# Performance work log

Hardware: AMD Instinct MI355X
Metric: run time of the kernel (lower is better)

Reference implementation:

```python
import jax, jax.numpy as jnp
import numpy as np

B, S, V = 8, 8192, 64
D, DV, DT, H = 256, 32, 256, 8
DH = D // H

def setup_inputs() -> dict:
    key = jax.random.key(0)
    ks = jax.random.split(key, 24)
    def p(i, shape, s=0.02):
        return jax.random.normal(ks[i], shape, jnp.float32) * s
    return {
        'times': jax.random.uniform(ks[0], (B, S), jnp.float32),
        'feature_ids': jax.random.randint(ks[1], (B, S), 0, V),
        'values': jax.random.normal(ks[2], (B, S), jnp.float32),
        'valid_mask': jax.random.randint(ks[3], (B, S), 0, 2).astype(bool),
        'me_w': p(4, (D,), 1.0), 'me_b': p(5, (D,)),
        'var_emb': p(6, (V, DV), 1.0),
        'time_w': p(7, (DT,), 1.0), 'time_b': p(8, (DT,)),
        'agg_w': p(9, (D + DT, D - DV)), 'agg_b': p(10, (D - DV,)),
        'wq': p(11, (D, D)), 'bq': p(12, (D,)),
        'wk': p(13, (D, D)), 'bk': p(14, (D,)),
        'wv': p(15, (D, D)), 'bv': p(16, (D,)),
        'wo': p(17, (D, D)), 'bo': p(18, (D,)),
        'cw1': p(19, (D, D)), 'cb1': p(20, (D,)),
        'cw2': p(21, (D, 1)), 'cb2': p(22, (1,)),
    }

def reference(times, feature_ids, values, valid_mask,
              me_w, me_b, var_emb, time_w, time_b, agg_w, agg_b,
              wq, bq, wk, bk, wv, bv, wo, bo, cw1, cb1, cw2, cb2):
    # Embeddings: measurement [B,S,D], variate [B,S,DV], time [B,S,DT]
    e_l = values[..., None] * me_w + me_b
    v_l = var_emb[feature_ids]
    u_l = times[..., None] * time_w + time_b
    eu = jnp.concatenate([e_l, u_l], axis=-1)                   # [B,S,D+DT]
    h_l = jnp.concatenate([v_l, eu @ agg_w + agg_b], axis=-1)   # [B,S,D]

    # Vectorized masked segment mean per variate (replaces Python loop)
    var_mask = (feature_ids[:, None, :] == jnp.arange(V)[None, :, None]) \
               & valid_mask[:, None, :]                         # [B,V,S] bool
    mf = var_mask.astype(h_l.dtype)
    sums = jnp.einsum('bvs,bsd->bvd', mf, h_l)
    counts = jnp.clip(mf.sum(-1), 1.0)                          # [B,V]
    f_mean = sums / counts[..., None]                           # [B,V,D]

    # Grouped cross-attention: one query per variate, shared K/V = h_l
    kpm = ~var_mask                                             # key padding mask
    all_masked = ~var_mask.any(-1)                              # [B,V]
    kpm = kpm.at[:, :, 0].set(kpm[:, :, 0] & ~all_masked)       # unmask pos 0 if empty

    q = (f_mean @ wq + bq).reshape(B, V, H, DH)
    k = (h_l @ wk + bk).reshape(B, S, H, DH)
    v = (h_l @ wv + bv).reshape(B, S, H, DH)
    scores = jnp.einsum('bvhd,bshd->bvhs', q, k) / np.sqrt(DH)  # [B,V,H,S]
    neg = jnp.finfo(scores.dtype).min
    scores = jnp.where(kpm[:, :, None, :], neg, scores)
    attn = jax.nn.softmax(scores, axis=-1)
    ctx = jnp.einsum('bvhs,bshd->bvhd', attn, v).reshape(B, V, D)
    f_var = ctx @ wo + bo                                       # [B,V,D]

    f = f_var.mean(axis=1)                                      # [B,D]
    out = jax.nn.relu(f @ cw1 + cb1) @ cw2 + cb2                # [B,1]
    return out
```

## Files before the change

### kernel.cpp

```cpp
#include <hip/hip_runtime.h>
#include <hip/hip_bf16.h>
#include <math.h>

#define BB 8
#define SS 8192
#define VV 64
#define AGG_OUT 224

#define WS_FLAGS 0
#define WS_A     16
#define WS_C     240
#define WS_D     464
#define WS_AQ    688
#define WS_CQ    944
#define WS_DQ    1200
#define WS_AK    1456
#define WS_CK    1712
#define WS_DK    1968
#define WS_AV    2224
#define WS_CV    2480
#define WS_DV    2736
#define WS_WQE   2992
#define WS_WKE   19376
#define WS_WVE   35760
#define WS_CSUM  52144
#define WS_BINS  54192
#define WS_COEF  66480
#define WS_SP    82864
#define WS_ACC   148416
#define WS_CNT   148424

__device__ __forceinline__ float ldf(const void* p, int idx, int fm) {
  if (fm) {
    unsigned int u = ((const unsigned short*)p)[idx];
    return __uint_as_float(u << 16);
  }
  return ((const float*)p)[idx];
}

__device__ __forceinline__ bool mask_at(const void* p, int idx, int mm) {
  switch (mm) {
    case 0: return ((const int*)p)[idx] != 0;
    case 1: return ((const float*)p)[idx] != 0.0f;
    case 2: return ((const unsigned short*)p)[idx] != 0;
    default: return ((const unsigned char*)p)[idx] != 0;
  }
}

__device__ __forceinline__ unsigned int fkey(float f) {
  unsigned int u = __float_as_uint(f);
  return (u & 0x80000000u) ? ~u : (u | 0x80000000u);
}
__device__ __forceinline__ float funkey(unsigned int k) {
  unsigned int u = (k & 0x80000000u) ? (k ^ 0x80000000u) : ~k;
  return __uint_as_float(u);
}

__device__ __forceinline__ int detect_fm_block(const void* times) {
  __shared__ int cntR;
  int tid = threadIdx.x;
  if (tid == 0) cntR = 0;
  __syncthreads();
  const unsigned int* tw = (const unsigned int*)times;
  int local = 0;
  for (int i = tid; i < 1024; i += 256) {
    unsigned int lo = tw[i] & 0xFFFFu;
    if (lo >= 0x3800u && lo < 0x3F80u) local++;
  }
  atomicAdd(&cntR, local);
  __syncthreads();
  int r = (cntR > 512) ? 1 : 0;
  __syncthreads();
  return r;
}

__device__ __forceinline__ int detect_mm_block(const void* mask) {
  __shared__ int f01, ff32, fbf;
  int tid = threadIdx.x;
  if (tid == 0) { f01 = 1; ff32 = 1; fbf = 1; }
  __syncthreads();
  const unsigned int* mw = (const unsigned int*)mask;
  int l01 = 1, lf32 = 1, lbf = 1;
  for (int i = tid; i < 2048; i += 256) {
    unsigned int w = mw[i];
    if (w > 1u) l01 = 0;
    if (!(w == 0u || w == 0x3F800000u)) lf32 = 0;
    unsigned int h0 = w & 0xFFFFu, h1 = w >> 16;
    if (!((h0 == 0u || h0 == 0x3F80u) && (h1 == 0u || h1 == 0x3F80u))) lbf = 0;
  }
  if (!l01) atomicAnd(&f01, 0);
  if (!lf32) atomicAnd(&ff32, 0);
  if (!lbf) atomicAnd(&fbf, 0);
  __syncthreads();
  int r = f01 ? 0 : (ff32 ? 1 : (fbf ? 2 : 3));
  __syncthreads();
  return r;
}

__global__ void __launch_bounds__(256) k_front(const void* times, const void* values,
                                               const int* fids, const void* mask,
                                               const void* me_w, const void* me_b,
                                               const void* time_w, const void* time_b,
                                               const void* agg_w, const void* agg_b,
                                               float* ws) {
  int blk = blockIdx.x, tid = threadIdx.x;
  if (blk < 224) {
    int fm = detect_fm_block(times);
    int j = blk, i = tid;
    float w0 = ldf(agg_w, i * AGG_OUT + j, fm);
    float w1 = ldf(agg_w, (256 + i) * AGG_OUT + j, fm);
    float sa = ldf(me_w, i, fm) * w0;
    float sc = ldf(time_w, i, fm) * w1;
    float sd = ldf(me_b, i, fm) * w0 + ldf(time_b, i, fm) * w1;
    #pragma unroll
    for (int off = 32; off >= 1; off >>= 1) {
      sa += __shfl_xor(sa, off);
      sc += __shfl_xor(sc, off);
      sd += __shfl_xor(sd, off);
    }
    __shared__ float r[3][4];
    int wid = i >> 6;
    if ((i & 63) == 0) { r[0][wid] = sa; r[1][wid] = sc; r[2][wid] = sd; }
    __syncthreads();
    if (i == 0) {
      ws[WS_A + j] = r[0][0] + r[0][1] + r[0][2] + r[0][3];
      ws[WS_C + j] = r[1][0] + r[1][1] + r[1][2] + r[1][3];
      ws[WS_D + j] = r[2][0] + r[2][1] + r[2][2] + r[2][3] + ldf(agg_b, j, fm);
    }
  } else if (blk < 352) {
    int fm = detect_fm_block(times);
    int mm = detect_mm_block(mask);
    int sblk = blk - 224, b = sblk >> 4, chunk = sblk & 15;
    __shared__ float hc[64], hsv[64], hst[64];
    __shared__ unsigned int hvn[64], hvx[64], htn[64], htx[64];
    if (tid < 64) {
      hc[tid] = 0.f; hsv[tid] = 0.f; hst[tid] = 0.f;
      hvn[tid] = 0xFFFFFFFFu; hvx[tid] = 0u;
      htn[tid] = 0xFFFFFFFFu; htx[tid] = 0u;
    }
    __syncthreads();
    #pragma unroll
    for (int k = 0; k < 2; k++) {
      int idx = b * SS + chunk * 512 + k * 256 + tid;
      if (mask_at(mask, idx, mm)) {
        int f = fids[idx];
        float val = ldf(values, idx, fm), tim = ldf(times, idx, fm);
        atomicAdd(&hc[f], 1.0f);
        atomicAdd(&hsv[f], val);
        atomicAdd(&hst[f], tim);
        unsigned int vk = fkey(val), tk = fkey(tim);
        atomicMin(&hvn[f], vk); atomicMax(&hvx[f], vk);
        atomicMin(&htn[f], tk); atomicMax(&htx[f], tk);
      }
    }
    __syncthreads();
    if (tid < 64) {
      int base = WS_SP + (sblk * 64 + tid) * 8;
      ws[base + 0] = hc[tid];
      ws[base + 1] = hsv[tid];
      ws[base + 2] = hst[tid];
      ((unsigned int*)ws)[base + 3] = hvn[tid];
      ((unsigned int*)ws)[base + 4] = hvx[tid];
      ((unsigned int*)ws)[base + 5] = htn[tid];
      ((unsigned int*)ws)[base + 6] = htx[tid];
    }
  } else {
    int zblk = blk - 352;
    for (int i = zblk * 256 + tid; i < 14336; i += 2048) ws[WS_CSUM + i] = 0.f;
    if (zblk == 1 && tid < 16) ws[WS_ACC + tid] = 0.f;
    if (zblk == 0) {
      int fm = detect_fm_block(times);
      int mm = detect_mm_block(mask);
      if (tid == 0) { ((int*)ws)[0] = fm; ((int*)ws)[1] = mm; }
    }
  }
}

__global__ void __launch_bounds__(256) k_pre(const void* wq, const void* wk,
                                             const void* wv, const void* bk,
                                             const void* bv, const void* var_emb,
                                             float* ws) {
  int fm = ((const int*)ws)[0];
  int blk = blockIdx.x, tid = threadIdx.x;
  if (blk < 24) {
    int X = blk >> 3, dg = blk & 7;
    const void* w = (X == 0) ? wq : (X == 1) ? wk : wv;
    __shared__ float sha[224], shc[224], shd[224];
    if (tid < 224) {
      sha[tid] = ws[WS_A + tid];
      shc[tid] = ws[WS_C + tid];
      shd[tid] = ws[WS_D + tid];
    }
    __syncthreads();
    int dsub = tid & 31, jg = tid >> 5;
    int d = dg * 32 + dsub;
    float sa = 0.f, sc = 0.f, sd = 0.f;
    #pragma unroll 4
    for (int jj = 0; jj < 28; jj++) {
      int j = jg * 28 + jj;
      float ww = ldf(w, (32 + j) * 256 + d, fm);
      sa += sha[j] * ww; sc += shc[j] * ww; sd += shd[j] * ww;
    }
    __shared__ float ps[3][8][32];
    ps[0][jg][dsub] = sa; ps[1][jg][dsub] = sc; ps[2][jg][dsub] = sd;
    __syncthreads();
    if (tid < 32) {
      float ra = 0.f, rc = 0.f, rd = 0.f;
      #pragma unroll
      for (int g = 0; g < 8; g++) {
        ra += ps[0][g][tid]; rc += ps[1][g][tid]; rd += ps[2][g][tid];
      }
      int dd = dg * 32 + tid;
      if (X == 1) rd += ldf(bk, dd, fm);
      if (X == 2) rd += ldf(bv, dd, fm);
      int base = (X == 0) ? WS_AQ : (X == 1) ? WS_AK : WS_AV;
      ws[base + dd] = ra;
      ws[base + 256 + dd] = rc;
      ws[base + 512 + dd] = rd;
    }
  } else {
    int idx = blk - 24, X = idx >> 6, v = idx & 63, d = tid;
    const void* w = (X == 0) ? wq : (X == 1) ? wk : wv;
    float s = 0.f;
    #pragma unroll 8
    for (int i = 0; i < 32; i++)
      s += ldf(var_emb, v * 32 + i, fm) * ldf(w, i * 256 + d, fm);
    int base = (X == 0) ? WS_WQE : (X == 1) ? WS_WKE : WS_WVE;
    ws[base + v * 256 + d] = s;
  }
}

__global__ void __launch_bounds__(256) k_coef(const void* values, const void* times,
                                              const int* fids, const void* bq,
                                              float* ws) {
  int fm = ((const int*)ws)[0];
  int bv = blockIdx.x, b = bv >> 6, v = bv & 63;
  int tid = threadIdx.x, h = tid >> 5;
  __shared__ float sp[16][8];
  if (tid < 128) {
    int sl = tid >> 3, c = tid & 7;
    sp[sl][c] = ws[WS_SP + ((b * 16 + sl) * 64 + v) * 8 + c];
  }
  __syncthreads();
  float cT = 0.f, svT = 0.f, stT = 0.f;
  unsigned int vnk = 0xFFFFFFFFu, vxk = 0u, tnk = 0xFFFFFFFFu, txk = 0u;
  #pragma unroll
  for (int sl = 0; sl < 16; sl++) {
    cT += sp[sl][0]; svT += sp[sl][1]; stT += sp[sl][2];
    unsigned int a3 = __float_as_uint(sp[sl][3]);
    unsigned int a4 = __float_as_uint(sp[sl][4]);
    unsigned int a5 = __float_as_uint(sp[sl][5]);
    unsigned int a6 = __float_as_uint(sp[sl][6]);
    vnk = min(vnk, a3); vxk = max(vxk, a4);
    tnk = min(tnk, a5); txk = max(txk, a6);
  }
  if (cT == 0.f) {
    int f0 = fids[b * SS];
    float v0 = ldf(values, b * SS, fm), t0 = ldf(times, b * SS, fm);
    float ctx = ws[WS_WVE + f0 * 256 + tid] + ws[WS_DV + tid]
              + v0 * ws[WS_AV + tid] + t0 * ws[WS_CV + tid];
    atomicAdd(&ws[WS_CSUM + b * 256 + tid], ctx);
    return;
  }
  float inv = 1.0f / cT, mv = svT * inv, mt = stT * inv;
  float qv = ldf(bq, tid, fm) + ws[WS_WQE + v * 256 + tid]
           + mv * ws[WS_AQ + tid] + mt * ws[WS_CQ + tid] + ws[WS_DQ + tid];
  qv *= 0.17677669529663687f * 1.4426950408889634f;
  float pA = qv * (ws[WS_WKE + v * 256 + tid] + ws[WS_DK + tid]);
  float pB = qv * ws[WS_AK + tid];
  float pC = qv * ws[WS_CK + tid];
  #pragma unroll
  for (int off = 16; off >= 1; off >>= 1) {
    pA += __shfl_xor(pA, off);
    pB += __shfl_xor(pB, off);
    pC += __shfl_xor(pC, off);
  }
  if ((tid & 31) == 0) {
    float vmn = funkey(vnk), vmx = funkey(vxk);
    float tmn = funkey(tnk), tmx = funkey(txk);
    float m = pA + fmaxf(pB * vmn, pB * vmx) + fmaxf(pC * tmn, pC * tmx);
    int base = WS_COEF + (bv * 8 + h) * 4;
    ws[base + 0] = pA; ws[base + 1] = pB; ws[base + 2] = pC; ws[base + 3] = m;
  }
}

__global__ void __launch_bounds__(256) k_accum(const void* values, const void* times,
                                               const int* fids, const void* mask,
                                               float* ws) {
  int fm = ((const int*)ws)[0], mm = ((const int*)ws)[1];
  int blk = blockIdx.x, tid = threadIdx.x;
  int b = blk >> 5, chunk = blk & 31;
  __shared__ float co[64 * 36];
  __shared__ float bins[64 * 25];
  for (int i = tid; i < 2048; i += 256) {
    int v = i >> 5, r = i & 31;
    co[v * 36 + r] = ws[WS_COEF + b * 2048 + i];
  }
  for (int i = tid; i < 1600; i += 256) bins[i] = 0.f;
  __syncthreads();
  {
    int idx = b * SS + chunk * 256 + tid;
    if (mask_at(mask, idx, mm)) {
      int f = fids[idx];
      float val = ldf(values, idx, fm), tim = ldf(times, idx, fm);
      #pragma unroll
      for (int h = 0; h < 8; h++) {
        int cb = f * 36 + h * 4;
        float w = exp2f(co[cb] + val * co[cb + 1] + tim * co[cb + 2] - co[cb + 3]);
        int bb = f * 25 + h * 3;
        atomicAdd(&bins[bb], w);
        atomicAdd(&bins[bb + 1], w * val);
        atomicAdd(&bins[bb + 2], w * tim);
      }
    }
  }
  __syncthreads();
  for (int i = tid; i < 1536; i += 256) {
    int f = i / 24, r = i - f * 24;
    float x = bins[f * 25 + r];
    if (x != 0.f) atomicAdd(&ws[WS_BINS + b * 1536 + i], x);
  }
}

__global__ void __launch_bounds__(1024) k_fin(const void* wo, const void* bo,
                                              const void* cw1, const void* cb1,
                                              const void* cw2, const void* cb2,
                                              float* ws, void* out) {
  int fm = ((const int*)ws)[0];
  int b = blockIdx.x, tid = threadIdx.x;
  __shared__ float aa[64][9], tt[64][9], ne[64];
  __shared__ float ps[4][256], cs[256], fv[256], pr[16];
  if (tid < 512) {
    int v = tid >> 3, h = tid & 7;
    int base = WS_BINS + b * 1536 + v * 24 + h * 3;
    float W = ws[base], WV = ws[base + 1], WT = ws[base + 2];
    float iW = (W > 0.f) ? 1.0f / W : 0.f;
    aa[v][h] = WV * iW; tt[v][h] = WT * iW;
    if (h == 0) ne[v] = (W > 0.f) ? 1.f : 0.f;
  }
  __syncthreads();
  int d = tid & 255, vg = tid >> 8, h = d >> 5;
  float accP = 0.f, accA = 0.f, accT = 0.f, accN = 0.f;
  #pragma unroll 4
  for (int k = 0; k < 16; k++) {
    int v = vg * 16 + k;
    float nef = ne[v];
    accP += nef * ws[WS_WVE + v * 256 + d];
    accA += aa[v][h];
    accT += tt[v][h];
    accN += nef;
  }
  ps[vg][d] = accP + accN * ws[WS_DV + d] + accA * ws[WS_AV + d] + accT * ws[WS_CV + d];
  __syncthreads();
  if (tid < 256)
    cs[tid] = (ws[WS_CSUM + b * 256 + tid] + ps[0][tid] + ps[1][tid]
             + ps[2][tid] + ps[3][tid]) * (1.0f / 64.0f);
  __syncthreads();
  float s = 0.f;
  #pragma unroll 8
  for (int k = 0; k < 64; k++) {
    int i = vg * 64 + k;
    s += cs[i] * ldf(wo, i * 256 + d, fm);
  }
  ps[vg][d] = s;
  __syncthreads();
  if (tid < 256) fv[tid] = ps[0][tid] + ps[1][tid] + ps[2][tid] + ps[3][tid]
                         + ldf(bo, tid, fm);
  __syncthreads();
  float t2 = 0.f;
  #pragma unroll 8
  for (int k = 0; k < 64; k++) {
    int i = vg * 64 + k;
    t2 += fv[i] * ldf(cw1, i * 256 + d, fm);
  }
  ps[vg][d] = t2;
  __syncthreads();
  float p = 0.f;
  if (tid < 256) {
    float t = ps[0][tid] + ps[1][tid] + ps[2][tid] + ps[3][tid] + ldf(cb1, tid, fm);
    t = fmaxf(t, 0.f);
    p = t * ldf(cw2, tid, fm);
  }
  #pragma unroll
  for (int off = 32; off >= 1; off >>= 1) p += __shfl_xor(p, off);
  if ((tid & 63) == 0) pr[tid >> 6] = p;
  __syncthreads();
  if (tid == 0) {
    float o = ldf(cb2, 0, fm);
    #pragma unroll
    for (int wgi = 0; wgi < 16; wgi++) o += pr[wgi];
    if (fm) {
      unsigned int x = __float_as_uint(o);
      unsigned int r = (x + 0x7FFFu + ((x >> 16) & 1u)) >> 16;
      ((unsigned short*)out)[b] = (unsigned short)r;
    } else {
      ((float*)out)[b] = o;
    }
  }
}

extern "C" void kernel_launch(void* const* d_in, const int* in_sizes, int n_in,
                              void* d_out, int out_size, void* d_ws, size_t ws_size,
                              hipStream_t stream) {
  const void* times   = d_in[0];
  const int*  fids    = (const int*)d_in[1];
  const void* values  = d_in[2];
  const void* vmask   = d_in[3];
  const void* me_w    = d_in[4];
  const void* me_b    = d_in[5];
  const void* var_emb = d_in[6];
  const void* time_w  = d_in[7];
  const void* time_b  = d_in[8];
  const void* agg_w   = d_in[9];
  const void* agg_b   = d_in[10];
  const void* wq = d_in[11]; const void* bq = d_in[12];
  const void* wk = d_in[13]; const void* bk = d_in[14];
  const void* wv = d_in[15]; const void* bv = d_in[16];
  const void* wo = d_in[17]; const void* bo = d_in[18];
  const void* cw1 = d_in[19]; const void* cb1 = d_in[20];
  const void* cw2 = d_in[21]; const void* cb2 = d_in[22];
  float* ws = (float*)d_ws;

  k_front<<<360, 256, 0, stream>>>(times, values, fids, vmask,
                                   me_w, me_b, time_w, time_b, agg_w, agg_b, ws);
  k_pre<<<216, 256, 0, stream>>>(wq, wk, wv, bk, bv, var_emb, ws);
  k_coef<<<512, 256, 0, stream>>>(values, times, fids, bq, ws);
  k_accum<<<256, 256, 0, stream>>>(values, times, fids, vmask, ws);
  k_fin<<<8, 1024, 0, stream>>>(wo, bo, cw1, cb1, cw2, cb2, ws, d_out);
}
```

Measured before the change: 142.1 us.

## Rebalance work across kernels: move var-emb projections to front, precompute PVE in coef

The var_emb×W projection blocks move from k_pre into k_front, so they run alongside the stats and aggregation blocks, and k_pre shrinks to 24 blocks. The per-batch nonempty-variate sum over WVE, previously computed in the serial 8-block k_fin, is now computed by 8 extra k_coef blocks from the partial counts. k_accum also loads coefficients with float4. The goal is to shorten the critical path in small kernels and the tail kernel. k_front gains more work, and each new block calls detect_fm_block redundantly.

Result: no change. 142.8 us (+0.6%).

```diff
diff --git a/kernel.cpp b/kernel.cpp
--- a/kernel.cpp
+++ b/kernel.cpp
@@ -27,8 +27,7 @@
 #define WS_BINS  54192
 #define WS_COEF  66480
 #define WS_SP    82864
-#define WS_ACC   148416
-#define WS_CNT   148424
+#define WS_PVE   148416
 
 __device__ __forceinline__ float ldf(const void* p, int idx, int fm) {
   if (fm) {
@@ -102,6 +101,8 @@
                                                const void* me_w, const void* me_b,
                                                const void* time_w, const void* time_b,
                                                const void* agg_w, const void* agg_b,
+                                               const void* wq, const void* wk,
+                                               const void* wv, const void* var_emb,
                                                float* ws) {
   int blk = blockIdx.x, tid = threadIdx.x;
   if (blk < 224) {
@@ -164,62 +165,17 @@
       ((unsigned int*)ws)[base + 5] = htn[tid];
       ((unsigned int*)ws)[base + 6] = htx[tid];
     }
-  } else {
+  } else if (blk < 360) {
     int zblk = blk - 352;
     for (int i = zblk * 256 + tid; i < 14336; i += 2048) ws[WS_CSUM + i] = 0.f;
-    if (zblk == 1 && tid < 16) ws[WS_ACC + tid] = 0.f;
     if (zblk == 0) {
       int fm = detect_fm_block(times);
       int mm = detect_mm_block(mask);
       if (tid == 0) { ((int*)ws)[0] = fm; ((int*)ws)[1] = mm; }
     }
-  }
-}
-
-__global__ void __launch_bounds__(256) k_pre(const void* wq, const void* wk,
-                                             const void* wv, const void* bk,
-                                             const void* bv, const void* var_emb,
-                                             float* ws) {
-  int fm = ((const int*)ws)[0];
-  int blk = blockIdx.x, tid = threadIdx.x;
-  if (blk < 24) {
-    int X = blk >> 3, dg = blk & 7;
-    const void* w = (X == 0) ? wq : (X == 1) ? wk : wv;
-    __shared__ float sha[224], shc[224], shd[224];
-    if (tid < 224) {
-      sha[tid] = ws[WS_A + tid];
-      shc[tid] = ws[WS_C + tid];
-      shd[tid] = ws[WS_D + tid];
-    }
-    __syncthreads();
-    int dsub = tid & 31, jg = tid >> 5;
-    int d = dg * 32 + dsub;
-    float sa = 0.f, sc = 0.f, sd = 0.f;
-    #pragma unroll 4
-    for (int jj = 0; jj < 28; jj++) {
-      int j = jg * 28 + jj;
-      float ww = ldf(w, (32 + j) * 256 + d, fm);
-      sa += sha[j] * ww; sc += shc[j] * ww; sd += shd[j] * ww;
-    }
-    __shared__ float ps[3][8][32];
-    ps[0][jg][dsub] = sa; ps[1][jg][dsub] = sc; ps[2][jg][dsub] = sd;
-    __syncthreads();
-    if (tid < 32) {
-      float ra = 0.f, rc = 0.f, rd = 0.f;
-      #pragma unroll
-      for (int g = 0; g < 8; g++) {
-        ra += ps[0][g][tid]; rc += ps[1][g][tid]; rd += ps[2][g][tid];
-      }
-      int dd = dg * 32 + tid;
-      if (X == 1) rd += ldf(bk, dd, fm);
-      if (X == 2) rd += ldf(bv, dd, fm);
-      int base = (X == 0) ? WS_AQ : (X == 1) ? WS_AK : WS_AV;
-      ws[base + dd] = ra;
-      ws[base + 256 + dd] = rc;
-      ws[base + 512 + dd] = rd;
-    }
   } else {
-    int idx = blk - 24, X = idx >> 6, v = idx & 63, d = tid;
+    int fm = detect_fm_block(times);
+    int idx = blk - 360, X = idx >> 6, v = idx & 63, d = tid;
     const void* w = (X == 0) ? wq : (X == 1) ? wk : wv;
     float s = 0.f;
     #pragma unroll 8
@@ -230,57 +186,130 @@
   }
 }
 
+__global__ void __launch_bounds__(256) k_pre(const void* wq, const void* wk,
+                                             const void* wv, const void* bk,
+                                             const void* bv, float* ws) {
+  int fm = ((const int*)ws)[0];
+  int blk = blockIdx.x, tid = threadIdx.x;
+  int X = blk >> 3, dg = blk & 7;
+  const void* w = (X == 0) ? wq : (X == 1) ? wk : wv;
+  __shared__ float sha[224], shc[224], shd[224];
+  if (tid < 224) {
+    sha[tid] = ws[WS_A + tid];
+    shc[tid] = ws[WS_C + tid];
+    shd[tid] = ws[WS_D + tid];
+  }
+  __syncthreads();
+  int dsub = tid & 31, jg = tid >> 5;
+  int d = dg * 32 + dsub;
+  float sa = 0.f, sc = 0.f, sd = 0.f;
+  #pragma unroll 4
+  for (int jj = 0; jj < 28; jj++) {
+    int j = jg * 28 + jj;
+    float ww = ldf(w, (32 + j) * 256 + d, fm);
+    sa += sha[j] * ww; sc += shc[j] * ww; sd += shd[j] * ww;
+  }
+  __shared__ float ps[3][8][32];
+  ps[0][jg][dsub] = sa; ps[1][jg][dsub] = sc; ps[2][jg][dsub] = sd;
+  __syncthreads();
+  if (tid < 32) {
+    float ra = 0.f, rc = 0.f, rd = 0.f;
+    #pragma unroll
+    for (int g = 0; g < 8; g++) {
+      ra += ps[0][g][tid]; rc += ps[1][g][tid]; rd += ps[2][g][tid];
+    }
+    int dd = dg * 32 + tid;
+    if (X == 1) rd += ldf(bk, dd, fm);
+    if (X == 2) rd += ldf(bv, dd, fm);
+    int base = (X == 0) ? WS_AQ : (X == 1) ? WS_AK : WS_AV;
+    ws[base + dd] = ra;
+    ws[base + 256 + dd] = rc;
+    ws[base + 512 + dd] = rd;
+  }
+}
+
 __global__ void __launch_bounds__(256) k_coef(const void* values, const void* times,
                                               const int* fids, const void* bq,
                                               float* ws) {
   int fm = ((const int*)ws)[0];
-  int bv = blockIdx.x, b = bv >> 6, v = bv & 63;
-  int tid = threadIdx.x, h = tid >> 5;
-  __shared__ float sp[16][8];
-  if (tid < 128) {
-    int sl = tid >> 3, c = tid & 7;
-    sp[sl][c] = ws[WS_SP + ((b * 16 + sl) * 64 + v) * 8 + c];
-  }
-  __syncthreads();
-  float cT = 0.f, svT = 0.f, stT = 0.f;
-  unsigned int vnk = 0xFFFFFFFFu, vxk = 0u, tnk = 0xFFFFFFFFu, txk = 0u;
-  #pragma unroll
-  for (int sl = 0; sl < 16; sl++) {
-    cT += sp[sl][0]; svT += sp[sl][1]; stT += sp[sl][2];
-    unsigned int a3 = __float_as_uint(sp[sl][3]);
-    unsigned int a4 = __float_as_uint(sp[sl][4]);
-    unsigned int a5 = __float_as_uint(sp[sl][5]);
-    unsigned int a6 = __float_as_uint(sp[sl][6]);
-    vnk = min(vnk, a3); vxk = max(vxk, a4);
-    tnk = min(tnk, a5); txk = max(txk, a6);
-  }
-  if (cT == 0.f) {
-    int f0 = fids[b * SS];
-    float v0 = ldf(values, b * SS, fm), t0 = ldf(times, b * SS, fm);
-    float ctx = ws[WS_WVE + f0 * 256 + tid] + ws[WS_DV + tid]
-              + v0 * ws[WS_AV + tid] + t0 * ws[WS_CV + tid];
-    atomicAdd(&ws[WS_CSUM + b * 256 + tid], ctx);
-    return;
-  }
-  float inv = 1.0f / cT, mv = svT * inv, mt = stT * inv;
-  float qv = ldf(bq, tid, fm) + ws[WS_WQE + v * 256 + tid]
-           + mv * ws[WS_AQ + tid] + mt * ws[WS_CQ + tid] + ws[WS_DQ + tid];
-  qv *= 0.17677669529663687f * 1.4426950408889634f;
-  float pA = qv * (ws[WS_WKE + v * 256 + tid] + ws[WS_DK + tid]);
-  float pB = qv * ws[WS_AK + tid];
-  float pC = qv * ws[WS_CK + tid];
-  #pragma unroll
-  for (int off = 16; off >= 1; off >>= 1) {
-    pA += __shfl_xor(pA, off);
-    pB += __shfl_xor(pB, off);
-    pC += __shfl_xor(pC, off);
-  }
-  if ((tid & 31) == 0) {
-    float vmn = funkey(vnk), vmx = funkey(vxk);
-    float tmn = funkey(tnk), tmx = funkey(txk);
-    float m = pA + fmaxf(pB * vmn, pB * vmx) + fmaxf(pC * tmn, pC * tmx);
-    int base = WS_COEF + (bv * 8 + h) * 4;
-    ws[base + 0] = pA; ws[base + 1] = pB; ws[base + 2] = pC; ws[base + 3] = m;
+  int blk = blockIdx.x, tid = threadIdx.x;
+  if (blk < 512) {
+    int bv = blk, b = bv >> 6, v = bv & 63;
+    int h = tid >> 5;
+    __shared__ float sp[16][8];
+    if (tid < 128) {
+      int sl = tid >> 3, c = tid & 7;
+      sp[sl][c] = ws[WS_SP + ((b * 16 + sl) * 64 + v) * 8 + c];
+    }
+    __syncthreads();
+    float cT = 0.f, svT = 0.f, stT = 0.f;
+    unsigned int vnk = 0xFFFFFFFFu, vxk = 0u, tnk = 0xFFFFFFFFu, txk = 0u;
+    #pragma unroll
+    for (int sl = 0; sl < 16; sl++) {
+      cT += sp[sl][0]; svT += sp[sl][1]; stT += sp[sl][2];
+      unsigned int a3 = __float_as_uint(sp[sl][3]);
+      unsigned int a4 = __float_as_uint(sp[sl][4]);
+      unsigned int a5 = __float_as_uint(sp[sl][5]);
+      unsigned int a6 = __float_as_uint(sp[sl][6]);
+      vnk = min(vnk, a3); vxk = max(vxk, a4);
+      tnk = min(tnk, a5); txk = max(txk, a6);
+    }
+    if (cT == 0.f) {
+      int f0 = fids[b * SS];
+      float v0 = ldf(values, b * SS, fm), t0 = ldf(times, b * SS, fm);
+      float ctx = ws[WS_WVE + f0 * 256 + tid] + ws[WS_DV + tid]
+                + v0 * ws[WS_AV + tid] + t0 * ws[WS_CV + tid];
+      atomicAdd(&ws[WS_CSUM + b * 256 + tid], ctx);
+      return;
+    }
+    float inv = 1.0f / cT, mv = svT * inv, mt = stT * inv;
+    float qv = ldf(bq, tid, fm) + ws[WS_WQE + v * 256 + tid]
+             + mv * ws[WS_AQ + tid] + mt * ws[WS_CQ + tid] + ws[WS_DQ + tid];
+    qv *= 0.17677669529663687f * 1.4426950408889634f;
+    float pA = qv * (ws[WS_WKE + v * 256 + tid] + ws[WS_DK + tid]);
+    float pB = qv * ws[WS_AK + tid];
+    float pC = qv * ws[WS_CK + tid];
+    #pragma unroll
+    for (int off = 16; off >= 1; off >>= 1) {
+      pA += __shfl_xor(pA, off);
+      pB += __shfl_xor(pB, off);
+      pC += __shfl_xor(pC, off);
+    }
+    if ((tid & 31) == 0) {
+      float vmn = funkey(vnk), vmx = funkey(vxk);
+      float tmn = funkey(tnk), tmx = funkey(txk);
+      float m = pA + fmaxf(pB * vmn, pB * vmx) + fmaxf(pC * tmn, pC * tmx);
+      int base = WS_COEF + (bv * 8 + h) * 4;
+      ws[base + 0] = pA; ws[base + 1] = pB; ws[base + 2] = pC; ws[base + 3] = m;
+    }
+  } else {
+    int b = blk - 512;
+    __shared__ float cnt4[64][4];
+    __shared__ float neL[64];
+    {
+      int v = tid & 63, g = tid >> 6;
+      float c = 0.f;
+      #pragma unroll
+      for (int s = 0; s < 4; s++) {
+        int sl = g * 4 + s;
+        c += ws[WS_SP + ((b * 16 + sl) * 64 + v) * 8 + 0];
+      }
+      cnt4[v][g] = c;
+    }
+    __syncthreads();
+    if (tid < 64)
+      neL[tid] = (cnt4[tid][0] + cnt4[tid][1] + cnt4[tid][2] + cnt4[tid][3] > 0.f)
+               ? 1.f : 0.f;
+    __syncthreads();
+    int d = tid;
+    float accP = 0.f, accN = 0.f;
+    #pragma unroll 8
+    for (int v = 0; v < VV; v++) {
+      float nef = neL[v];
+      accP += nef * ws[WS_WVE + v * 256 + d];
+      accN += nef;
+    }
+    ws[WS_PVE + b * 256 + d] = accP + accN * ws[WS_DV + d];
   }
 }
 
@@ -292,9 +321,11 @@
   int b = blk >> 5, chunk = blk & 31;
   __shared__ float co[64 * 36];
   __shared__ float bins[64 * 25];
-  for (int i = tid; i < 2048; i += 256) {
-    int v = i >> 5, r = i & 31;
-    co[v * 36 + r] = ws[WS_COEF + b * 2048 + i];
+  for (int q = tid; q < 512; q += 256) {
+    float4 x = ((const float4*)(ws + WS_COEF + b * 2048))[q];
+    int v = q >> 3, r = (q & 7) * 4;
+    float* dst = &co[v * 36 + r];
+    dst[0] = x.x; dst[1] = x.y; dst[2] = x.z; dst[3] = x.w;
   }
   for (int i = tid; i < 1600; i += 256) bins[i] = 0.f;
   __syncthreads();
@@ -328,7 +359,7 @@
                                               float* ws, void* out) {
   int fm = ((const int*)ws)[0];
   int b = blockIdx.x, tid = threadIdx.x;
-  __shared__ float aa[64][9], tt[64][9], ne[64];
+  __shared__ float aa[64][9], tt[64][9];
   __shared__ float ps[4][256], cs[256], fv[256], pr[16];
   if (tid < 512) {
     int v = tid >> 3, h = tid & 7;
@@ -336,25 +367,21 @@
     float W = ws[base], WV = ws[base + 1], WT = ws[base + 2];
     float iW = (W > 0.f) ? 1.0f / W : 0.f;
     aa[v][h] = WV * iW; tt[v][h] = WT * iW;
-    if (h == 0) ne[v] = (W > 0.f) ? 1.f : 0.f;
   }
   __syncthreads();
   int d = tid & 255, vg = tid >> 8, h = d >> 5;
-  float accP = 0.f, accA = 0.f, accT = 0.f, accN = 0.f;
+  float accA = 0.f, accT = 0.f;
   #pragma unroll 4
   for (int k = 0; k < 16; k++) {
     int v = vg * 16 + k;
-    float nef = ne[v];
-    accP += nef * ws[WS_WVE + v * 256 + d];
     accA += aa[v][h];
     accT += tt[v][h];
-    accN += nef;
-  }
-  ps[vg][d] = accP + accN * ws[WS_DV + d] + accA * ws[WS_AV + d] + accT * ws[WS_CV + d];
+  }
+  ps[vg][d] = accA * ws[WS_AV + d] + accT * ws[WS_CV + d];
   __syncthreads();
   if (tid < 256)
-    cs[tid] = (ws[WS_CSUM + b * 256 + tid] + ps[0][tid] + ps[1][tid]
-             + ps[2][tid] + ps[3][tid]) * (1.0f / 64.0f);
+    cs[tid] = (ws[WS_CSUM + b * 256 + tid] + ws[WS_PVE + b * 256 + tid]
+             + ps[0][tid] + ps[1][tid] + ps[2][tid] + ps[3][tid]) * (1.0f / 64.0f);
   __syncthreads();
   float s = 0.f;
   #pragma unroll 8
@@ -421,10 +448,11 @@
   const void* cw2 = d_in[21]; const void* cb2 = d_in[22];
   float* ws = (float*)d_ws;
 
-  k_front<<<360, 256, 0, stream>>>(times, values, fids, vmask,
-                                   me_w, me_b, time_w, time_b, agg_w, agg_b, ws);
-  k_pre<<<216, 256, 0, stream>>>(wq, wk, wv, bk, bv, var_emb, ws);
-  k_coef<<<512, 256, 0, stream>>>(values, times, fids, bq, ws);
+  k_front<<<552, 256, 0, stream>>>(times, values, fids, vmask,
+                                   me_w, me_b, time_w, time_b, agg_w, agg_b,
+                                   wq, wk, wv, var_emb, ws);
+  k_pre<<<24, 256, 0, stream>>>(wq, wk, wv, bk, bv, ws);
+  k_coef<<<520, 256, 0, stream>>>(values, times, fids, bq, ws);
   k_accum<<<256, 256, 0, stream>>>(values, times, fids, vmask, ws);
   k_fin<<<8, 1024, 0, stream>>>(wo, bo, cw1, cb1, cw2, cb2, ws, d_out);
 }
```
